# Optimization experiments

Measured on AMD Instinct MI355X. Metric: run time of the kernel, lower is better.

## Reference

```python
import jax, jax.numpy as jnp
import numpy as np

EPS_COV = 0.01  # module eps added to covariance diagonal
G, N_MEM = 8, 64  # groups, channels per group


def _pade_coeffs(m=5):
    # Taylor coefficients of sqrt(1 - x): c_k = (-1)^k * binom(1/2, k)
    c = np.zeros(2 * m + 1)
    c[0] = 1.0
    b = 1.0
    for k in range(1, 2 * m + 1):
        b *= (0.5 - (k - 1)) / k
        c[k] = ((-1) ** k) * b
    # Pade [m/m]: q_0 = 1, solve sum_j q_j c_{k-j} = 0 for k = m+1..2m
    A = np.zeros((m, m))
    rhs = np.zeros(m)
    for i in range(m):
        k = m + 1 + i
        for j in range(m):
            A[i, j] = c[k - (j + 1)]
        rhs[i] = -c[k]
    q = np.concatenate([[1.0], np.linalg.solve(A, rhs)])
    p = np.array([sum(q[j] * c[k - j] for j in range(min(k, m) + 1)) for k in range(m + 1)])
    return p, q

_PADE_P, _PADE_Q = _pade_coeffs(5)


def matrix_pade_approximant(p, I):
    # evaluates the [5/5] Pade approximant of sqrt at p (normalized SPD matrix)
    pp = jnp.asarray(_PADE_P, dtype=p.dtype)
    pq = jnp.asarray(_PADE_Q, dtype=p.dtype)
    p_app = I - p
    p_sqrt = pp[0] * I
    q_sqrt = pq[0] * I
    p_hat = p_app
    for i in range(5):
        p_sqrt = p_sqrt + pp[i + 1] * p_hat
        q_sqrt = q_sqrt + pq[i + 1] * p_hat
        p_hat = p_hat @ p_app
    return jnp.linalg.solve(q_sqrt, p_sqrt)


def mpa_sqrt(M):
    # batched matrix square root via Pade approximant (MPA_Lya.forward)
    normM = jnp.linalg.norm(M, axis=(1, 2))[:, None, None]
    n = M.shape[1]
    I = jnp.broadcast_to(jnp.eye(n, dtype=M.dtype), M.shape)
    return matrix_pade_approximant(M / normM, I) * jnp.sqrt(normM)


def setup_inputs() -> dict:
    key = jax.random.key(0)
    k1, k2 = jax.random.split(key)
    x = jax.random.normal(k1, (32, 512, 64, 64), dtype=jnp.float32)
    weight = jax.random.uniform(k2, (G, N_MEM, 1), dtype=jnp.float32)
    bias = jnp.zeros((G, N_MEM, 1), dtype=jnp.float32)
    return {"x": x, "weight": weight, "bias": bias}


def reference(x, weight, bias):
    N, C, H, W = x.shape
    n_mem = C // G
    xg = jnp.transpose(x, (1, 0, 2, 3)).reshape(G, n_mem, -1)  # (G, n_mem, N*H*W)
    mu = jnp.mean(xg, axis=2, keepdims=True)
    xg = xg - mu
    I = jnp.eye(n_mem, dtype=x.dtype)[None]
    xxt = jnp.einsum('gim,gjm->gij', xg, xg) / (N * H * W) + I * EPS_COV
    subspace = jnp.linalg.inv(mpa_sqrt(xxt))  # ZCA whitening matrix per group
    xr = jnp.einsum('gij,gjm->gim', subspace, xg)
    xr = xr * weight + bias
    xr = xr.reshape(C, N, H, W)
    return jnp.transpose(xr, (1, 0, 2, 3))
```

## Files before the change

kernel.cpp:

```cpp
#include <hip/hip_runtime.h>

#define NBATCH 32
#define CHAN   512
#define HWSZ   4096
#define NG     8
#define NM     64
#define MTOT   (NBATCH * HWSZ)
#define EPSC   0.01f
#define P68    68

typedef _Float16 f16;
typedef _Float16 f16x8 __attribute__((ext_vector_type(8)));
typedef float    f32x4 __attribute__((ext_vector_type(4)));

#define MFMA16(a, b, c) __builtin_amdgcn_mfma_f32_16x16x32_f16(a, b, c, 0, 0, 0)

__global__ __launch_bounds__(256) void gram_k(const float* __restrict__ x,
                                              float* __restrict__ gpart,
                                              float* __restrict__ spart) {
    __shared__ float red[2][4096];
    __shared__ float wsum[4][64];

    const int bid  = blockIdx.x;
    const int g    = bid >> 6;
    const int n    = (bid >> 1) & 31;
    const int half = bid & 1;
    const float* xb = x + ((size_t)(n * CHAN + g * NM)) * HWSZ + half * 2048;

    const int t = threadIdx.x;
    const int w = t >> 6;
    const int l = t & 63;

    const float* base = xb + (size_t)(l & 15) * HWSZ + w * 32 + (l >> 4) * 8;

    f32x4 acc[4][4];
#pragma unroll
    for (int i = 0; i < 4; ++i)
#pragma unroll
        for (int j = 0; j < 4; ++j) acc[i][j] = (f32x4){0.f, 0.f, 0.f, 0.f};
    float fs[4] = {0.f, 0.f, 0.f, 0.f};

    for (int tt = 0; tt < 16; ++tt) {
        const float* bt = base + tt * 128;
        f16x8 frag[4];
#pragma unroll
        for (int rb = 0; rb < 4; ++rb) {
            const float* pr = bt + (size_t)rb * 16 * HWSZ;
            const float4 v0 = *(const float4*)pr;
            const float4 v1 = *(const float4*)(pr + 4);
            fs[rb] += (v0.x + v0.y) + (v0.z + v0.w) + (v1.x + v1.y) + (v1.z + v1.w);
            f16x8 hv;
            hv[0] = (f16)v0.x; hv[1] = (f16)v0.y; hv[2] = (f16)v0.z; hv[3] = (f16)v0.w;
            hv[4] = (f16)v1.x; hv[5] = (f16)v1.y; hv[6] = (f16)v1.z; hv[7] = (f16)v1.w;
            frag[rb] = hv;
        }
#pragma unroll
        for (int i = 0; i < 4; ++i)
#pragma unroll
            for (int j = 0; j < 4; ++j)
                acc[i][j] = MFMA16(frag[i], frag[j], acc[i][j]);
    }

#pragma unroll
    for (int rb = 0; rb < 4; ++rb) {
        fs[rb] += __shfl_xor(fs[rb], 16);
        fs[rb] += __shfl_xor(fs[rb], 32);
    }
    if (l < 16) {
#pragma unroll
        for (int rb = 0; rb < 4; ++rb) wsum[w][rb * 16 + l] = fs[rb];
    }
    __syncthreads();
    if (t < 64)
        spart[(size_t)bid * 64 + t] =
            (wsum[0][t] + wsum[1][t]) + (wsum[2][t] + wsum[3][t]);

    if (w >= 2) {
#pragma unroll
        for (int i = 0; i < 4; ++i)
#pragma unroll
            for (int j = 0; j < 4; ++j)
#pragma unroll
                for (int r = 0; r < 4; ++r) {
                    const int row = i * 16 + (l >> 4) * 4 + r;
                    const int col = j * 16 + (l & 15);
                    red[w - 2][row * 64 + col] = acc[i][j][r];
                }
    }
    __syncthreads();
    if (w < 2) {
#pragma unroll
        for (int i = 0; i < 4; ++i)
#pragma unroll
            for (int j = 0; j < 4; ++j)
#pragma unroll
                for (int r = 0; r < 4; ++r) {
                    const int row = i * 16 + (l >> 4) * 4 + r;
                    const int col = j * 16 + (l & 15);
                    red[w][row * 64 + col] += acc[i][j][r];
                }
    }
    __syncthreads();
#pragma unroll
    for (int k = 0; k < 16; ++k) {
        const int e = t + 256 * k;
        gpart[(size_t)bid * 4096 + e] = red[0][e] + red[1][e];
    }
}

__global__ __launch_bounds__(256) void reduce_k(const float* __restrict__ gpart,
                                                const float* __restrict__ spart,
                                                float* __restrict__ gram,
                                                float* __restrict__ sums) {
    const int g = blockIdx.x >> 4, c = blockIdx.x & 15;
    const int t = threadIdx.x;
    float s = 0.f;
    for (int p = 0; p < 64; ++p)
        s += gpart[((size_t)(g * 64 + p)) * 4096 + c * 256 + t];
    gram[g * 4096 + c * 256 + t] = s;
    if (c == 0 && t < 64) {
        float ss = 0.f;
        for (int p = 0; p < 64; ++p) ss += spart[(size_t)(g * 64 + p) * 64 + t];
        sums[g * 64 + t] = ss;
    }
}

__global__ __launch_bounds__(256) void solve_k(const float* __restrict__ gram,
                                               const float* __restrict__ sums,
                                               const float* __restrict__ wgt,
                                               const float* __restrict__ bias,
                                               f16* __restrict__ Tf,
                                               float* __restrict__ offv) {
    __shared__ __align__(16) float A[64 * P68];
    __shared__ __align__(16) float B[64 * P68];
    __shared__ __align__(16) float Cc[64 * P68];
    __shared__ __align__(16) float Dd[64 * P68];
    __shared__ float mus[64];
    __shared__ float red[4];
    __shared__ float tr16[16];

    const int g = blockIdx.x, t = threadIdx.x;
    const float* gg = gram + g * 4096;

    if (t < 64) mus[t] = sums[g * NM + t] * (1.0f / MTOT);
    __syncthreads();

    float covv[16];
    float loc = 0.f;
#pragma unroll
    for (int k = 0; k < 16; ++k) {
        const int e = t + 256 * k;
        const int i = e >> 6, j = e & 63;
        const float cv = gg[e] * (1.0f / MTOT) - mus[i] * mus[j] + (i == j ? EPSC : 0.f);
        covv[k] = cv;
        loc += cv * cv;
    }
#pragma unroll
    for (int o = 32; o > 0; o >>= 1) loc += __shfl_down(loc, o);
    if ((t & 63) == 0) red[t >> 6] = loc;
    __syncthreads();
    const float normM = sqrtf(red[0] + red[1] + red[2] + red[3]);
    const float ninv  = 1.0f / normM;

#pragma unroll
    for (int k = 0; k < 16; ++k) {
        const int e = t + 256 * k;
        const int i = e >> 6, j = e & 63;
        const float pa = (i == j ? 1.f : 0.f) - covv[k] * ninv;
        A[i * P68 + j] = pa;
        B[i * P68 + j] = pa;
    }
    __syncthreads();

    const int ty = t >> 4, tx = t & 15;
    const int i0 = ty * 4, j0 = tx * 4;

    const float PP[6] = {1.f, -2.75f, 2.75f, -1.203125f, 0.21484375f, -0.0107421875f};
    const float QQ[6] = {1.f, -2.25f, 1.75f, -0.546875f, 0.05859375f, -0.0009765625f};

    float pacc[4][4], qacc[4][4];
#pragma unroll
    for (int ai = 0; ai < 4; ++ai)
#pragma unroll
        for (int bi = 0; bi < 4; ++bi) {
            const int i = i0 + ai, j = j0 + bi;
            const float pa = A[i * P68 + j];
            const float id = (i == j) ? 1.f : 0.f;
            pacc[ai][bi] = PP[0] * id + PP[1] * pa;
            qacc[ai][bi] = QQ[0] * id + QQ[1] * pa;
        }

    float* src = B;
    float* dst = Cc;
    for (int s = 0; s < 4; ++s) {
        float mm[4][4];
#pragma unroll
        for (int ai = 0; ai < 4; ++ai)
#pragma unroll
            for (int bi = 0; bi < 4; ++bi) mm[ai][bi] = 0.f;
        for (int kk = 0; kk < 64; ++kk) {
            const float4 a4 = *(const float4*)&src[kk * P68 + i0];
            const float4 b4 = *(const float4*)&A[kk * P68 + j0];
            const float av[4] = {a4.x, a4.y, a4.z, a4.w};
            const float bv[4] = {b4.x, b4.y, b4.z, b4.w};
#pragma unroll
            for (int ai = 0; ai < 4; ++ai)
#pragma unroll
                for (int bi = 0; bi < 4; ++bi)
                    mm[ai][bi] = fmaf(av[ai], bv[bi], mm[ai][bi]);
        }
#pragma unroll
        for (int ai = 0; ai < 4; ++ai) {
            float4 w4;
            w4.x = mm[ai][0]; w4.y = mm[ai][1]; w4.z = mm[ai][2]; w4.w = mm[ai][3];
            *(float4*)&dst[(i0 + ai) * P68 + j0] = w4;
        }
#pragma unroll
        for (int ai = 0; ai < 4; ++ai)
#pragma unroll
            for (int bi = 0; bi < 4; ++bi) {
                pacc[ai][bi] = fmaf(PP[s + 2], mm[ai][bi], pacc[ai][bi]);
                qacc[ai][bi] = fmaf(QQ[s + 2], mm[ai][bi], qacc[ai][bi]);
            }
        __syncthreads();
        float* tmpp = src; src = dst; dst = tmpp;
    }

    if (ty == tx)
        tr16[tx] = pacc[0][0] + pacc[1][1] + pacc[2][2] + pacc[3][3];
    __syncthreads();
    float trsum = 0.f;
#pragma unroll
    for (int i = 0; i < 16; ++i) trsum += tr16[i];
    const float cP  = trsum * (1.0f / 64.0f);
    const float icP = 1.0f / cP;

#pragma unroll
    for (int ai = 0; ai < 4; ++ai) {
        float4 we, wq;
        const int i = i0 + ai;
        we.x = pacc[ai][0] * icP - (i == j0 + 0 ? 1.f : 0.f);
        we.y = pacc[ai][1] * icP - (i == j0 + 1 ? 1.f : 0.f);
        we.z = pacc[ai][2] * icP - (i == j0 + 2 ? 1.f : 0.f);
        we.w = pacc[ai][3] * icP - (i == j0 + 3 ? 1.f : 0.f);
        wq.x = qacc[ai][0]; wq.y = qacc[ai][1]; wq.z = qacc[ai][2]; wq.w = qacc[ai][3];
        *(float4*)&A[i * P68 + j0] = we;
        *(float4*)&B[i * P68 + j0] = wq;
    }
    __syncthreads();

    float* rsrc = B;
    float* rdst = Cc;
    for (int it = 0; it < 6; ++it) {
        float mm[4][4];
#pragma unroll
        for (int ai = 0; ai < 4; ++ai)
#pragma unroll
            for (int bi = 0; bi < 4; ++bi) mm[ai][bi] = 0.f;
        for (int kk = 0; kk < 64; ++kk) {
            const float4 a4 = *(const float4*)&A[kk * P68 + i0];
            const float4 b4 = *(const float4*)&rsrc[kk * P68 + j0];
            const float av[4] = {a4.x, a4.y, a4.z, a4.w};
            const float bv[4] = {b4.x, b4.y, b4.z, b4.w};
#pragma unroll
            for (int ai = 0; ai < 4; ++ai)
#pragma unroll
                for (int bi = 0; bi < 4; ++bi)
                    mm[ai][bi] = fmaf(av[ai], bv[bi], mm[ai][bi]);
        }
#pragma unroll
        for (int ai = 0; ai < 4; ++ai) {
            const float4 q4 = *(const float4*)&B[(i0 + ai) * P68 + j0];
            float4 w4;
            w4.x = q4.x - mm[ai][0]; w4.y = q4.y - mm[ai][1];
            w4.z = q4.z - mm[ai][2]; w4.w = q4.w - mm[ai][3];
            *(float4*)&rdst[(i0 + ai) * P68 + j0] = w4;
        }
        __syncthreads();
        if (it == 0) { rsrc = Cc; rdst = Dd; }
        else { float* tmpp = rsrc; rsrc = rdst; rdst = tmpp; }
    }
    float* X = rsrc;

    const float invs = icP / sqrtf(normM);
    if (t < 64) {
        float sm = 0.f;
        for (int j = 0; j < 64; ++j) sm += X[t * P68 + j] * mus[j];
        offv[g * NM + t] = bias[g * NM + t] - sm * invs * wgt[g * NM + t];
    }
#pragma unroll
    for (int k = 0; k < 16; ++k) {
        const int e = t + 256 * k;
        const int i = e >> 6, j = e & 63;
        Tf[(size_t)g * 4096 + e] = (f16)(X[i * P68 + j] * invs * wgt[g * NM + i]);
    }
}

__global__ __launch_bounds__(256) void apply_k(const float* __restrict__ x,
                                               const f16* __restrict__ Tf,
                                               const float* __restrict__ offv,
                                               float* __restrict__ out) {
    __shared__ __align__(16) f16 xs[2][128 * 64];
    __shared__ __align__(16) f16 Ts[4096];
    __shared__ float offs[64];

    const int bid  = blockIdx.x;
    const int g    = bid >> 6;
    const int n    = (bid >> 1) & 31;
    const int half = bid & 1;
    const size_t base = ((size_t)(n * CHAN + g * NM)) * HWSZ + half * 2048;
    const float* xb = x + base;
    float* ob = out + base;

    const int t = threadIdx.x;
    const int w = t >> 6;
    const int l = t & 63;

#pragma unroll
    for (int i = 0; i < 2; ++i) {
        const int c   = t + 256 * i;
        const int oc  = c >> 3;
        const int icb = (c & 7) * 8;
        const f16x8 v = *(const f16x8*)&Tf[(size_t)g * 4096 + oc * 64 + icb];
        *(f16x8*)&Ts[oc * 64 + (icb ^ ((oc & 7) << 3))] = v;
    }
    if (t < 64) offs[t] = offv[g * NM + t];

    const int chS   = t >> 4;
    const int off8S = (t & 15) * 8;

    {
        const float* xt = xb;
#pragma unroll
        for (int i = 0; i < 4; ++i) {
            const int ch = chS + 16 * i;
            const float4 v0 = *(const float4*)(xt + (size_t)ch * HWSZ + off8S);
            const float4 v1 = *(const float4*)(xt + (size_t)ch * HWSZ + off8S + 4);
            f16 h[8];
            h[0] = (f16)v0.x; h[1] = (f16)v0.y; h[2] = (f16)v0.z; h[3] = (f16)v0.w;
            h[4] = (f16)v1.x; h[5] = (f16)v1.y; h[6] = (f16)v1.z; h[7] = (f16)v1.w;
#pragma unroll
            for (int j = 0; j < 8; ++j) {
                const int pos = off8S + j;
                xs[0][pos * 64 + (ch ^ (((pos ^ (pos >> 3)) & 7) << 3))] = h[j];
            }
        }
    }
    __syncthreads();

    f16x8 afrag[2];
#pragma unroll
    for (int c = 0; c < 2; ++c) {
        const int oc = w * 16 + (l & 15);
        const int k0 = c * 32 + (l >> 4) * 8;
        afrag[c] = *(const f16x8*)&Ts[oc * 64 + (k0 ^ ((oc & 7) << 3))];
    }
    float offr[4];
#pragma unroll
    for (int r = 0; r < 4; ++r) offr[r] = offs[w * 16 + (l >> 4) * 4 + r];

    for (int tt = 0; tt < 16; ++tt) {
        const int cur = tt & 1;

        float4 va[4][2];
        if (tt < 15) {
            const float* xt = xb + (tt + 1) * 128;
#pragma unroll
            for (int i = 0; i < 4; ++i) {
                const int ch = chS + 16 * i;
                va[i][0] = *(const float4*)(xt + (size_t)ch * HWSZ + off8S);
                va[i][1] = *(const float4*)(xt + (size_t)ch * HWSZ + off8S + 4);
            }
        }

#pragma unroll
        for (int pb = 0; pb < 8; ++pb) {
            f32x4 acc;
            acc[0] = offr[0]; acc[1] = offr[1]; acc[2] = offr[2]; acc[3] = offr[3];
            const int pos = pb * 16 + (l & 15);
            const int swz = ((pos ^ (pos >> 3)) & 7) << 3;
#pragma unroll
            for (int c = 0; c < 2; ++c) {
                const int k0 = c * 32 + (l >> 4) * 8;
                const f16x8 bfrag = *(const f16x8*)&xs[cur][pos * 64 + (k0 ^ swz)];
                acc = MFMA16(afrag[c], bfrag, acc);
            }
            const int posg = tt * 128 + pb * 16 + (l & 15);
#pragma unroll
            for (int r = 0; r < 4; ++r) {
                const int oc = w * 16 + (l >> 4) * 4 + r;
                ob[(size_t)oc * HWSZ + posg] = acc[r];
            }
        }

        if (tt < 15) {
#pragma unroll
            for (int i = 0; i < 4; ++i) {
                const int ch = chS + 16 * i;
                f16 h[8];
                h[0] = (f16)va[i][0].x; h[1] = (f16)va[i][0].y;
                h[2] = (f16)va[i][0].z; h[3] = (f16)va[i][0].w;
                h[4] = (f16)va[i][1].x; h[5] = (f16)va[i][1].y;
                h[6] = (f16)va[i][1].z; h[7] = (f16)va[i][1].w;
#pragma unroll
                for (int j = 0; j < 8; ++j) {
                    const int pos = off8S + j;
                    xs[cur ^ 1][pos * 64 + (ch ^ (((pos ^ (pos >> 3)) & 7) << 3))] = h[j];
                }
            }
        }
        __syncthreads();
    }
}

extern "C" void kernel_launch(void* const* d_in, const int* in_sizes, int n_in,
                              void* d_out, int out_size, void* d_ws, size_t ws_size,
                              hipStream_t stream) {
    const float* x    = (const float*)d_in[0];
    const float* wgt  = (const float*)d_in[1];
    const float* bias = (const float*)d_in[2];
    float* out = (float*)d_out;

    float* ws    = (float*)d_ws;
    float* gpart = ws;
    float* spart = ws + 2097152;
    float* gram  = ws + 2129920;
    float* sums  = ws + 2162688;
    float* offv  = ws + 2163200;
    f16*   Tf    = (f16*)(ws + 2163712);

    gram_k  <<<512, 256, 0, stream>>>(x, gpart, spart);
    reduce_k<<<128, 256, 0, stream>>>(gpart, spart, gram, sums);
    solve_k <<<8,   256, 0, stream>>>(gram, sums, wgt, bias, Tf, offv);
    apply_k <<<512, 256, 0, stream>>>(x, Tf, offv, out);
}
```

Before: 252.7 us.

## Split spatial work into quarters and drop apply double buffering

Both gram_k and apply_k now split each (group, batch) slab into four spatial quarters instead of two, doubling the grid to 1024 blocks so more of the GPU's compute units are occupied. reduce_k sums 128 partials per group, and the workspace offsets grow to hold them. apply_k replaces its register-prefetched double-buffered LDS pipeline with a single buffer loaded synchronously each iteration. This halves LDS use for higher occupancy but gives up in-block overlap of loads with MFMA work and adds a barrier per tile. The larger partial Gram buffer also means more reduction traffic.

```diff
diff --git a/kernel.cpp b/kernel.cpp
--- a/kernel.cpp
+++ b/kernel.cpp
@@ -22,10 +22,11 @@
     __shared__ float wsum[4][64];
 
     const int bid  = blockIdx.x;
-    const int g    = bid >> 6;
-    const int n    = (bid >> 1) & 31;
-    const int half = bid & 1;
-    const float* xb = x + ((size_t)(n * CHAN + g * NM)) * HWSZ + half * 2048;
+    const int g    = bid >> 7;
+    const int rest = bid & 127;
+    const int n    = rest >> 2;
+    const int q    = rest & 3;
+    const float* xb = x + ((size_t)(n * CHAN + g * NM)) * HWSZ + q * 1024;
 
     const int t = threadIdx.x;
     const int w = t >> 6;
@@ -40,7 +41,7 @@
         for (int j = 0; j < 4; ++j) acc[i][j] = (f32x4){0.f, 0.f, 0.f, 0.f};
     float fs[4] = {0.f, 0.f, 0.f, 0.f};
 
-    for (int tt = 0; tt < 16; ++tt) {
+    for (int tt = 0; tt < 8; ++tt) {
         const float* bt = base + tt * 128;
         f16x8 frag[4];
 #pragma unroll
@@ -115,12 +116,12 @@
     const int g = blockIdx.x >> 4, c = blockIdx.x & 15;
     const int t = threadIdx.x;
     float s = 0.f;
-    for (int p = 0; p < 64; ++p)
-        s += gpart[((size_t)(g * 64 + p)) * 4096 + c * 256 + t];
+    for (int p = 0; p < 128; ++p)
+        s += gpart[((size_t)(g * 128 + p)) * 4096 + c * 256 + t];
     gram[g * 4096 + c * 256 + t] = s;
     if (c == 0 && t < 64) {
         float ss = 0.f;
-        for (int p = 0; p < 64; ++p) ss += spart[(size_t)(g * 64 + p) * 64 + t];
+        for (int p = 0; p < 128; ++p) ss += spart[(size_t)(g * 128 + p) * 64 + t];
         sums[g * 64 + t] = ss;
     }
 }
@@ -300,15 +301,16 @@
                                                const f16* __restrict__ Tf,
                                                const float* __restrict__ offv,
                                                float* __restrict__ out) {
-    __shared__ __align__(16) f16 xs[2][128 * 64];
+    __shared__ __align__(16) f16 xs[128 * 64];
     __shared__ __align__(16) f16 Ts[4096];
     __shared__ float offs[64];
 
     const int bid  = blockIdx.x;
-    const int g    = bid >> 6;
-    const int n    = (bid >> 1) & 31;
-    const int half = bid & 1;
-    const size_t base = ((size_t)(n * CHAN + g * NM)) * HWSZ + half * 2048;
+    const int g    = bid >> 7;
+    const int rest = bid & 127;
+    const int n    = rest >> 2;
+    const int q    = rest & 3;
+    const size_t base = ((size_t)(n * CHAN + g * NM)) * HWSZ + q * 1024;
     const float* xb = x + base;
     float* ob = out + base;
 
@@ -325,27 +327,6 @@
         *(f16x8*)&Ts[oc * 64 + (icb ^ ((oc & 7) << 3))] = v;
     }
     if (t < 64) offs[t] = offv[g * NM + t];
-
-    const int chS   = t >> 4;
-    const int off8S = (t & 15) * 8;
-
-    {
-        const float* xt = xb;
-#pragma unroll
-        for (int i = 0; i < 4; ++i) {
-            const int ch = chS + 16 * i;
-            const float4 v0 = *(const float4*)(xt + (size_t)ch * HWSZ + off8S);
-            const float4 v1 = *(const float4*)(xt + (size_t)ch * HWSZ + off8S + 4);
-            f16 h[8];
-            h[0] = (f16)v0.x; h[1] = (f16)v0.y; h[2] = (f16)v0.z; h[3] = (f16)v0.w;
-            h[4] = (f16)v1.x; h[5] = (f16)v1.y; h[6] = (f16)v1.z; h[7] = (f16)v1.w;
-#pragma unroll
-            for (int j = 0; j < 8; ++j) {
-                const int pos = off8S + j;
-                xs[0][pos * 64 + (ch ^ (((pos ^ (pos >> 3)) & 7) << 3))] = h[j];
-            }
-        }
-    }
     __syncthreads();
 
     f16x8 afrag[2];
@@ -359,19 +340,26 @@
 #pragma unroll
     for (int r = 0; r < 4; ++r) offr[r] = offs[w * 16 + (l >> 4) * 4 + r];
 
-    for (int tt = 0; tt < 16; ++tt) {
-        const int cur = tt & 1;
-
-        float4 va[4][2];
-        if (tt < 15) {
-            const float* xt = xb + (tt + 1) * 128;
-#pragma unroll
-            for (int i = 0; i < 4; ++i) {
-                const int ch = chS + 16 * i;
-                va[i][0] = *(const float4*)(xt + (size_t)ch * HWSZ + off8S);
-                va[i][1] = *(const float4*)(xt + (size_t)ch * HWSZ + off8S + 4);
+    for (int tt = 0; tt < 8; ++tt) {
+        const float* xt = xb + tt * 128;
+        __syncthreads();
+#pragma unroll
+        for (int i = 0; i < 4; ++i) {
+            const int p    = t + 256 * i;
+            const int ch   = p >> 4;
+            const int off8 = (p & 15) * 8;
+            const float4 v0 = *(const float4*)(xt + (size_t)ch * HWSZ + off8);
+            const float4 v1 = *(const float4*)(xt + (size_t)ch * HWSZ + off8 + 4);
+            f16 h[8];
+            h[0] = (f16)v0.x; h[1] = (f16)v0.y; h[2] = (f16)v0.z; h[3] = (f16)v0.w;
+            h[4] = (f16)v1.x; h[5] = (f16)v1.y; h[6] = (f16)v1.z; h[7] = (f16)v1.w;
+#pragma unroll
+            for (int j = 0; j < 8; ++j) {
+                const int pos = off8 + j;
+                xs[pos * 64 + (ch ^ (((pos ^ (pos >> 3)) & 7) << 3))] = h[j];
             }
         }
+        __syncthreads();
 
 #pragma unroll
         for (int pb = 0; pb < 8; ++pb) {
@@ -382,7 +370,7 @@
 #pragma unroll
             for (int c = 0; c < 2; ++c) {
                 const int k0 = c * 32 + (l >> 4) * 8;
-                const f16x8 bfrag = *(const f16x8*)&xs[cur][pos * 64 + (k0 ^ swz)];
+                const f16x8 bfrag = *(const f16x8*)&xs[pos * 64 + (k0 ^ swz)];
                 acc = MFMA16(afrag[c], bfrag, acc);
             }
             const int posg = tt * 128 + pb * 16 + (l & 15);
@@ -392,24 +380,6 @@
                 ob[(size_t)oc * HWSZ + posg] = acc[r];
             }
         }
-
-        if (tt < 15) {
-#pragma unroll
-            for (int i = 0; i < 4; ++i) {
-                const int ch = chS + 16 * i;
-                f16 h[8];
-                h[0] = (f16)va[i][0].x; h[1] = (f16)va[i][0].y;
-                h[2] = (f16)va[i][0].z; h[3] = (f16)va[i][0].w;
-                h[4] = (f16)va[i][1].x; h[5] = (f16)va[i][1].y;
-                h[6] = (f16)va[i][1].z; h[7] = (f16)va[i][1].w;
-#pragma unroll
-                for (int j = 0; j < 8; ++j) {
-                    const int pos = off8S + j;
-                    xs[cur ^ 1][pos * 64 + (ch ^ (((pos ^ (pos >> 3)) & 7) << 3))] = h[j];
-                }
-            }
-        }
-        __syncthreads();
     }
 }
 
@@ -423,14 +393,14 @@
 
     float* ws    = (float*)d_ws;
     float* gpart = ws;
-    float* spart = ws + 2097152;
-    float* gram  = ws + 2129920;
-    float* sums  = ws + 2162688;
-    float* offv  = ws + 2163200;
-    f16*   Tf    = (f16*)(ws + 2163712);
-
-    gram_k  <<<512, 256, 0, stream>>>(x, gpart, spart);
-    reduce_k<<<128, 256, 0, stream>>>(gpart, spart, gram, sums);
-    solve_k <<<8,   256, 0, stream>>>(gram, sums, wgt, bias, Tf, offv);
-    apply_k <<<512, 256, 0, stream>>>(x, Tf, offv, out);
+    float* spart = ws + 4194304;
+    float* gram  = ws + 4259840;
+    float* sums  = ws + 4292608;
+    float* offv  = ws + 4293120;
+    f16*   Tf    = (f16*)(ws + 4293632);
+
+    gram_k  <<<1024, 256, 0, stream>>>(x, gpart, spart);
+    reduce_k<<<128,  256, 0, stream>>>(gpart, spart, gram, sums);
+    solve_k <<<8,    256, 0, stream>>>(gram, sums, wgt, bias, Tf, offv);
+    apply_k <<<1024, 256, 0, stream>>>(x, Tf, offv, out);
 }
```

After: 288.7 us. +14.2%, slower.
